# Kernel optimization log

Hardware: AMD Instinct MI355X
Metric: run time of the kernel (lower is better)

Reference implementation:

```python
import jax, jax.numpy as jnp
import numpy as np

# Uniform batched-graph layout: B graphs, each with N_PER nodes and E_PER edges.
# Graph g owns nodes [g*N_PER, (g+1)*N_PER) and edges [g*E_PER, (g+1)*E_PER).
B = 256
N_PER = 512
E_PER = 4096
D = 64               # emb_dim
RATIO = 0.25
K = int(RATIO * E_PER)  # edges reserved per graph (causal)


def setup_inputs() -> dict:
    key = jax.random.key(0)
    k_h, k_src, k_dst, k_w1, k_w2 = jax.random.split(key, 5)
    h = jax.random.normal(k_h, (B * N_PER, D), dtype=jnp.float32)
    # edge endpoints local to each graph, then offset into the global node space
    src = jax.random.randint(k_src, (B, E_PER), 0, N_PER, dtype=jnp.int32)
    dst = jax.random.randint(k_dst, (B, E_PER), 0, N_PER, dtype=jnp.int32)
    offs = (jnp.arange(B, dtype=jnp.int32) * N_PER)[:, None]
    edge_index = jnp.stack([(src + offs).reshape(-1), (dst + offs).reshape(-1)])  # [2, B*E_PER]
    batch = jnp.repeat(jnp.arange(B, dtype=jnp.int32), N_PER)  # node -> graph id
    W1 = jax.random.normal(k_w1, (2 * D, 4 * D), dtype=jnp.float32) / np.sqrt(2 * D)
    b1 = jnp.zeros((4 * D,), dtype=jnp.float32)
    W2 = jax.random.normal(k_w2, (4 * D, 1), dtype=jnp.float32) / np.sqrt(4 * D)
    b2 = jnp.zeros((1,), dtype=jnp.float32)
    return {"h": h, "W1": W1, "b1": b1, "W2": W2, "b2": b2,
            "edge_index": edge_index, "batch": batch}


def reference(h, W1, b1, W2, b2, edge_index, batch):
    row, col = edge_index[0], edge_index[1]
    # edge attention MLP: Linear(2D->4D) -> ReLU -> Linear(4D->1)
    edge_rep = jnp.concatenate([h[row], h[col]], axis=-1)          # [E, 2D]
    scores = (jax.nn.relu(edge_rep @ W1 + b1) @ W2 + b2)[:, 0]     # [E] pred_edge_weight

    # segmented top-k per graph (replaces the per-graph CPU argpartition loop)
    s = scores.reshape(B, E_PER)
    order = jnp.argsort(-s, axis=1)                                # descending
    keep = order[:, :K]                                            # causal edge slots
    drop = order[:, K:]                                            # spurious edge slots
    goff = (jnp.arange(B, dtype=keep.dtype) * E_PER)[:, None]
    keep_g = (keep + goff).reshape(-1)                             # [B*K] global edge ids
    drop_g = (drop + goff).reshape(-1)                             # [B*(E_PER-K)]
    causal_edge_weight = scores[keep_g]
    spu_edge_weight = -scores[drop_g]

    # relabel + 'feat' branch with c_pool='add': nodes touched by causal edges,
    # global_add_pool of their embeddings per graph (compaction is index-preserving math)
    ce_row = row[keep_g]
    ce_col = col[keep_g]
    node_mask = jnp.zeros((h.shape[0],), dtype=bool)
    node_mask = node_mask.at[ce_row].set(True).at[ce_col].set(True)
    causal_rep = jax.ops.segment_sum(
        jnp.where(node_mask[:, None], h, jnp.zeros((), h.dtype)),
        batch, num_segments=B)                                     # [B, D]

    return causal_rep, causal_edge_weight, spu_edge_weight
```

## Files before the change

kernel.cpp:

```cpp
#include <hip/hip_runtime.h>
#include <stdint.h>

#define B_GRAPHS 256
#define NPER     512
#define EPER     4096
#define DDIM     64
#define KKEEP    1024
#define HIDDEN   256
#define CT       16
#define NTILE    (HIDDEN/CT)
#define STR      20

__global__ __launch_bounds__(1024) void scores_kernel(
    const float* __restrict__ h, const float* __restrict__ W1,
    const float* __restrict__ b1, const float* __restrict__ W2,
    const float* __restrict__ b2, const int* __restrict__ edge0,
    const int* __restrict__ edge1, float* __restrict__ sc_out)
{
  __shared__ __align__(16) float At[NPER * STR];
  __shared__ __align__(16) float Bt[NPER * STR];
  const int t  = threadIdx.x;
  const int b  = blockIdx.x;
  const int n  = t & (NPER - 1);
  const int ch = __builtin_amdgcn_readfirstlane(t >> 9);

  int epk[4];
  float eacc[4];
#pragma unroll
  for (int i = 0; i < 4; ++i) {
    const size_t e = (size_t)b * EPER + t + i * 1024;
    epk[i] = (edge0[e] & (NPER - 1)) | ((edge1[e] & (NPER - 1)) << 16);
    eacc[i] = 0.f;
  }

  const float* __restrict__ hrow = h + ((size_t)b * NPER + n) * DDIM;

  for (int jt = 0; jt < NTILE; ++jt) {
    const int j0 = jt * CT;
    const int jc = j0 + ch * 8;

    asm volatile("" ::: "memory");

    float pa[8], pb[8];
#pragma unroll
    for (int jj = 0; jj < 8; ++jj) { pa[jj] = b1[jc + jj]; pb[jj] = 0.f; }

#pragma unroll
    for (int dc = 0; dc < 4; ++dc) {
      const float4* hp = (const float4*)(hrow + dc * 16);
      float4 h0 = hp[0], h1 = hp[1], h2 = hp[2], h3 = hp[3];
      float hc[16];
      hc[0]=h0.x; hc[1]=h0.y; hc[2]=h0.z; hc[3]=h0.w;
      hc[4]=h1.x; hc[5]=h1.y; hc[6]=h1.z; hc[7]=h1.w;
      hc[8]=h2.x; hc[9]=h2.y; hc[10]=h2.z; hc[11]=h2.w;
      hc[12]=h3.x; hc[13]=h3.y; hc[14]=h3.z; hc[15]=h3.w;
#pragma unroll
      for (int k = 0; k < 16; ++k) {
        const int d = dc * 16 + k;
        const float hv = hc[k];
#pragma unroll
        for (int jj = 0; jj < 8; ++jj)
          pa[jj] = fmaf(hv, W1[d * HIDDEN + jc + jj], pa[jj]);
#pragma unroll
        for (int jj = 0; jj < 8; ++jj)
          pb[jj] = fmaf(hv, W1[(DDIM + d) * HIDDEN + jc + jj], pb[jj]);
      }
    }

    {
      float* ap = At + n * STR + ch * 8;
      float* bp = Bt + n * STR + ch * 8;
      float4 s0 = {pa[0], pa[1], pa[2], pa[3]};
      float4 s1 = {pa[4], pa[5], pa[6], pa[7]};
      ((float4*)ap)[0] = s0; ((float4*)ap)[1] = s1;
      float4 u0 = {pb[0], pb[1], pb[2], pb[3]};
      float4 u1 = {pb[4], pb[5], pb[6], pb[7]};
      ((float4*)bp)[0] = u0; ((float4*)bp)[1] = u1;
    }
    __syncthreads();

    float w2r[CT];
#pragma unroll
    for (int jj = 0; jj < CT; ++jj) w2r[jj] = W2[j0 + jj];

#pragma unroll
    for (int i = 0; i < 4; ++i) {
      const int er = epk[i] & 0xffff;
      const int ec = ((unsigned)epk[i]) >> 16;
      const float4* ar = (const float4*)(At + er * STR);
      const float4* br = (const float4*)(Bt + ec * STR);
      float p = 0.f;
#pragma unroll
      for (int q = 0; q < 4; ++q) {
        const float4 a = ar[q], c = br[q];
        p = fmaf(fmaxf(a.x + c.x, 0.f), w2r[4*q+0], p);
        p = fmaf(fmaxf(a.y + c.y, 0.f), w2r[4*q+1], p);
        p = fmaf(fmaxf(a.z + c.z, 0.f), w2r[4*q+2], p);
        p = fmaf(fmaxf(a.w + c.w, 0.f), w2r[4*q+3], p);
      }
      eacc[i] += p;
    }
    __syncthreads();
  }

  const float b2v = b2[0];
#pragma unroll
  for (int i = 0; i < 4; ++i)
    sc_out[(size_t)b * EPER + t + i * 1024] = eacc[i] + b2v;
}

__global__ __launch_bounds__(1024) void sort_kernel(
    const float* __restrict__ sc, const int* __restrict__ edge0,
    const int* __restrict__ edge1, const float* __restrict__ h,
    float* __restrict__ out_rep, float* __restrict__ out_cw,
    float* __restrict__ out_sw)
{
  __shared__ unsigned long long keys[EPER];
  __shared__ int mask[NPER];
  __shared__ float red[16 * 64];
  const int t = threadIdx.x;
  const int b = blockIdx.x;

  if (t < NPER) mask[t] = 0;

#pragma unroll
  for (int i = 0; i < 4; ++i) {
    const int e = t + i * 1024;
    const float s = sc[(size_t)b * EPER + e];
    unsigned u  = __float_as_uint(s);
    unsigned fk = (u & 0x80000000u) ? ~u : (u | 0x80000000u);
    unsigned dk = ~fk;
    keys[e] = ((unsigned long long)dk << 32) | (unsigned)e;
  }

  for (int k = 2; k <= EPER; k <<= 1) {
    for (int j = k >> 1; j > 0; j >>= 1) {
      __syncthreads();
#pragma unroll
      for (int i = 0; i < 4; ++i) {
        const int p = t + i * 1024;
        const int l = p ^ j;
        if (l > p) {
          const unsigned long long a = keys[p], c = keys[l];
          const bool up = ((p & k) == 0);
          if (up ? (a > c) : (a < c)) { keys[p] = c; keys[l] = a; }
        }
      }
    }
  }
  __syncthreads();

#pragma unroll
  for (int i = 0; i < 4; ++i) {
    const int p = t + i * 1024;
    const unsigned long long key = keys[p];
    const unsigned fk = ~(unsigned)(key >> 32);
    const unsigned u  = (fk & 0x80000000u) ? (fk & 0x7fffffffu) : ~fk;
    const float s = __uint_as_float(u);
    if (p < KKEEP) out_cw[(size_t)b * KKEEP + p] = s;
    else           out_sw[(size_t)b * (EPER - KKEEP) + (p - KKEEP)] = -s;
  }

  {
    const int e = (int)(keys[t] & 0xffffffffu);
    const size_t eg = (size_t)b * EPER + e;
    mask[edge0[eg] & (NPER - 1)] = 1;
    mask[edge1[eg] & (NPER - 1)] = 1;
  }
  __syncthreads();

  {
    const int d = t & 63, g = t >> 6;
    float s = 0.f;
    for (int nn = g; nn < NPER; nn += 16)
      if (mask[nn]) s += h[((size_t)b * NPER + nn) * DDIM + d];
    red[g * 64 + d] = s;
  }
  __syncthreads();
  if (t < 64) {
    float tot = 0.f;
#pragma unroll
    for (int g = 0; g < 16; ++g) tot += red[g * 64 + t];
    out_rep[(size_t)b * DDIM + t] = tot;
  }
}

extern "C" void kernel_launch(void* const* d_in, const int* in_sizes, int n_in,
                              void* d_out, int out_size, void* d_ws, size_t ws_size,
                              hipStream_t stream) {
  const float* h    = (const float*)d_in[0];
  const float* W1   = (const float*)d_in[1];
  const float* b1   = (const float*)d_in[2];
  const float* W2   = (const float*)d_in[3];
  const float* b2   = (const float*)d_in[4];
  const int*   eidx = (const int*)d_in[5];
  const int* edge0 = eidx;
  const int* edge1 = eidx + (size_t)B_GRAPHS * EPER;

  float* sc = (float*)d_ws;

  float* out     = (float*)d_out;
  float* out_rep = out;
  float* out_cw  = out + B_GRAPHS * DDIM;
  float* out_sw  = out_cw + (size_t)B_GRAPHS * KKEEP;

  scores_kernel<<<B_GRAPHS, 1024, 0, stream>>>(h, W1, b1, W2, b2, edge0, edge1, sc);
  sort_kernel<<<B_GRAPHS, 1024, 0, stream>>>(sc, edge0, edge1, h, out_rep, out_cw, out_sw);
}
```

Baseline: 335.4 us.

## Warp-specialize score kernel into producer/consumer roles with double-buffered LDS

The 1024-thread block now splits into two roles. Threads 0-511 compute node projections for an 8-wide hidden tile into one of two LDS buffers, while threads 512-1023 consume the previous tile to accumulate edge scores for 8 edges each. This aims to overlap the projection FMAs with the LDS gather/ReLU work and halve the barriers per tile. In exchange each role does twice as many tiles or edges serially, and the number of pipeline ticks doubles, so per-role work and latency could rise.

```diff
diff --git a/kernel.cpp b/kernel.cpp
--- a/kernel.cpp
+++ b/kernel.cpp
@@ -7,9 +7,9 @@
 #define DDIM     64
 #define KKEEP    1024
 #define HIDDEN   256
-#define CT       16
-#define NTILE    (HIDDEN/CT)
-#define STR      20
+#define CT       8
+#define NTICK    (HIDDEN/CT)
+#define STR      12
 
 __global__ __launch_bounds__(1024) void scores_kernel(
     const float* __restrict__ h, const float* __restrict__ W1,
@@ -17,96 +17,99 @@
     const float* __restrict__ b2, const int* __restrict__ edge0,
     const int* __restrict__ edge1, float* __restrict__ sc_out)
 {
-  __shared__ __align__(16) float At[NPER * STR];
-  __shared__ __align__(16) float Bt[NPER * STR];
-  const int t  = threadIdx.x;
-  const int b  = blockIdx.x;
-  const int n  = t & (NPER - 1);
-  const int ch = __builtin_amdgcn_readfirstlane(t >> 9);
-
-  int epk[4];
-  float eacc[4];
-#pragma unroll
-  for (int i = 0; i < 4; ++i) {
-    const size_t e = (size_t)b * EPER + t + i * 1024;
-    epk[i] = (edge0[e] & (NPER - 1)) | ((edge1[e] & (NPER - 1)) << 16);
-    eacc[i] = 0.f;
+  __shared__ __align__(16) float At[2][NPER * STR];
+  __shared__ __align__(16) float Bt[2][NPER * STR];
+  const int t    = threadIdx.x;
+  const int b    = blockIdx.x;
+  const int role = __builtin_amdgcn_readfirstlane(t >> 9);
+  const int n    = t & (NPER - 1);
+
+  int epk[8];
+  float eacc[8];
+  if (role) {
+#pragma unroll
+    for (int i = 0; i < 8; ++i) {
+      const size_t e = (size_t)b * EPER + n + i * 512;
+      epk[i]  = (edge0[e] & (NPER - 1)) | ((edge1[e] & (NPER - 1)) << 16);
+      eacc[i] = 0.f;
+    }
   }
 
   const float* __restrict__ hrow = h + ((size_t)b * NPER + n) * DDIM;
 
-  for (int jt = 0; jt < NTILE; ++jt) {
-    const int j0 = jt * CT;
-    const int jc = j0 + ch * 8;
-
-    asm volatile("" ::: "memory");
-
-    float pa[8], pb[8];
-#pragma unroll
-    for (int jj = 0; jj < 8; ++jj) { pa[jj] = b1[jc + jj]; pb[jj] = 0.f; }
-
-#pragma unroll
-    for (int dc = 0; dc < 4; ++dc) {
-      const float4* hp = (const float4*)(hrow + dc * 16);
-      float4 h0 = hp[0], h1 = hp[1], h2 = hp[2], h3 = hp[3];
-      float hc[16];
-      hc[0]=h0.x; hc[1]=h0.y; hc[2]=h0.z; hc[3]=h0.w;
-      hc[4]=h1.x; hc[5]=h1.y; hc[6]=h1.z; hc[7]=h1.w;
-      hc[8]=h2.x; hc[9]=h2.y; hc[10]=h2.z; hc[11]=h2.w;
-      hc[12]=h3.x; hc[13]=h3.y; hc[14]=h3.z; hc[15]=h3.w;
-#pragma unroll
-      for (int k = 0; k < 16; ++k) {
-        const int d = dc * 16 + k;
-        const float hv = hc[k];
-#pragma unroll
-        for (int jj = 0; jj < 8; ++jj)
-          pa[jj] = fmaf(hv, W1[d * HIDDEN + jc + jj], pa[jj]);
-#pragma unroll
-        for (int jj = 0; jj < 8; ++jj)
-          pb[jj] = fmaf(hv, W1[(DDIM + d) * HIDDEN + jc + jj], pb[jj]);
+  for (int jt = 0; jt <= NTICK; ++jt) {
+    if (role == 0) {
+      if (jt < NTICK) {
+        const int jc = jt * CT;
+        asm volatile("" ::: "memory");
+        float pa[CT], pb[CT];
+#pragma unroll
+        for (int jj = 0; jj < CT; ++jj) { pa[jj] = b1[jc + jj]; pb[jj] = 0.f; }
+#pragma unroll
+        for (int dc = 0; dc < 4; ++dc) {
+          const float4* hp = (const float4*)(hrow + dc * 16);
+          const float4 h0 = hp[0], h1 = hp[1], h2 = hp[2], h3 = hp[3];
+          const float hc[16] = {h0.x,h0.y,h0.z,h0.w, h1.x,h1.y,h1.z,h1.w,
+                                h2.x,h2.y,h2.z,h2.w, h3.x,h3.y,h3.z,h3.w};
+#pragma unroll
+          for (int k = 0; k < 16; ++k) {
+            const int d = dc * 16 + k;
+            const float hv = hc[k];
+#pragma unroll
+            for (int jj = 0; jj < CT; ++jj)
+              pa[jj] = fmaf(hv, W1[d * HIDDEN + jc + jj], pa[jj]);
+#pragma unroll
+            for (int jj = 0; jj < CT; ++jj)
+              pb[jj] = fmaf(hv, W1[(DDIM + d) * HIDDEN + jc + jj], pb[jj]);
+          }
+        }
+        const int p = jt & 1;
+        float4 s0 = {pa[0], pa[1], pa[2], pa[3]};
+        float4 s1 = {pa[4], pa[5], pa[6], pa[7]};
+        ((float4*)(At[p] + n * STR))[0] = s0;
+        ((float4*)(At[p] + n * STR))[1] = s1;
+        float4 u0 = {pb[0], pb[1], pb[2], pb[3]};
+        float4 u1 = {pb[4], pb[5], pb[6], pb[7]};
+        ((float4*)(Bt[p] + n * STR))[0] = u0;
+        ((float4*)(Bt[p] + n * STR))[1] = u1;
+      }
+    } else {
+      if (jt >= 1) {
+        const int jc = (jt - 1) * CT;
+        const int p  = (jt - 1) & 1;
+        float w2r[CT];
+#pragma unroll
+        for (int jj = 0; jj < CT; ++jj) w2r[jj] = W2[jc + jj];
+#pragma unroll
+        for (int i = 0; i < 8; ++i) {
+          const int er = epk[i] & 0xffff;
+          const int ec = ((unsigned)epk[i]) >> 16;
+          const float4* ar = (const float4*)(At[p] + er * STR);
+          const float4* br = (const float4*)(Bt[p] + ec * STR);
+          const float4 a0 = ar[0], a1 = ar[1];
+          const float4 c0 = br[0], c1 = br[1];
+          float q = 0.f;
+          q = fmaf(fmaxf(a0.x + c0.x, 0.f), w2r[0], q);
+          q = fmaf(fmaxf(a0.y + c0.y, 0.f), w2r[1], q);
+          q = fmaf(fmaxf(a0.z + c0.z, 0.f), w2r[2], q);
+          q = fmaf(fmaxf(a0.w + c0.w, 0.f), w2r[3], q);
+          q = fmaf(fmaxf(a1.x + c1.x, 0.f), w2r[4], q);
+          q = fmaf(fmaxf(a1.y + c1.y, 0.f), w2r[5], q);
+          q = fmaf(fmaxf(a1.z + c1.z, 0.f), w2r[6], q);
+          q = fmaf(fmaxf(a1.w + c1.w, 0.f), w2r[7], q);
+          eacc[i] += q;
+        }
       }
     }
-
-    {
-      float* ap = At + n * STR + ch * 8;
-      float* bp = Bt + n * STR + ch * 8;
-      float4 s0 = {pa[0], pa[1], pa[2], pa[3]};
-      float4 s1 = {pa[4], pa[5], pa[6], pa[7]};
-      ((float4*)ap)[0] = s0; ((float4*)ap)[1] = s1;
-      float4 u0 = {pb[0], pb[1], pb[2], pb[3]};
-      float4 u1 = {pb[4], pb[5], pb[6], pb[7]};
-      ((float4*)bp)[0] = u0; ((float4*)bp)[1] = u1;
-    }
     __syncthreads();
-
-    float w2r[CT];
-#pragma unroll
-    for (int jj = 0; jj < CT; ++jj) w2r[jj] = W2[j0 + jj];
-
-#pragma unroll
-    for (int i = 0; i < 4; ++i) {
-      const int er = epk[i] & 0xffff;
-      const int ec = ((unsigned)epk[i]) >> 16;
-      const float4* ar = (const float4*)(At + er * STR);
-      const float4* br = (const float4*)(Bt + ec * STR);
-      float p = 0.f;
-#pragma unroll
-      for (int q = 0; q < 4; ++q) {
-        const float4 a = ar[q], c = br[q];
-        p = fmaf(fmaxf(a.x + c.x, 0.f), w2r[4*q+0], p);
-        p = fmaf(fmaxf(a.y + c.y, 0.f), w2r[4*q+1], p);
-        p = fmaf(fmaxf(a.z + c.z, 0.f), w2r[4*q+2], p);
-        p = fmaf(fmaxf(a.w + c.w, 0.f), w2r[4*q+3], p);
-      }
-      eacc[i] += p;
-    }
-    __syncthreads();
-  }
-
-  const float b2v = b2[0];
-#pragma unroll
-  for (int i = 0; i < 4; ++i)
-    sc_out[(size_t)b * EPER + t + i * 1024] = eacc[i] + b2v;
+  }
+
+  if (role) {
+    const float b2v = b2[0];
+#pragma unroll
+    for (int i = 0; i < 8; ++i)
+      sc_out[(size_t)b * EPER + n + i * 512] = eacc[i] + b2v;
+  }
 }
 
 __global__ __launch_bounds__(1024) void sort_kernel(
```

After: 362.2 us. 1.08x slower.

## Double-buffer hidden-column tiles and halve tile width in scores kernel

Applied to the files above, without the earlier changes.

Splits the hidden dimension into 8-column tiles instead of 16 and double-buffers the per-node partial projections in shared memory. Each iteration computes the next tile while the edges consume the previous one, so only one barrier per iteration remains instead of two. The cost is twice as many tile iterations, each reloading h rows and doing fewer FMAs, and a smaller per-thread register tile.

```diff
diff --git a/kernel.cpp b/kernel.cpp
--- a/kernel.cpp
+++ b/kernel.cpp
@@ -7,9 +7,11 @@
 #define DDIM     64
 #define KKEEP    1024
 #define HIDDEN   256
-#define CT       16
+#define CT       8
 #define NTILE    (HIDDEN/CT)
-#define STR      20
+#define STR      12
+
+typedef unsigned long long u64;
 
 __global__ __launch_bounds__(1024) void scores_kernel(
     const float* __restrict__ h, const float* __restrict__ W1,
@@ -17,8 +19,8 @@
     const float* __restrict__ b2, const int* __restrict__ edge0,
     const int* __restrict__ edge1, float* __restrict__ sc_out)
 {
-  __shared__ __align__(16) float At[NPER * STR];
-  __shared__ __align__(16) float Bt[NPER * STR];
+  __shared__ __align__(16) float At[2][NPER * STR];
+  __shared__ __align__(16) float Bt[2][NPER * STR];
   const int t  = threadIdx.x;
   const int b  = blockIdx.x;
   const int n  = t & (NPER - 1);
@@ -35,71 +37,73 @@
 
   const float* __restrict__ hrow = h + ((size_t)b * NPER + n) * DDIM;
 
-  for (int jt = 0; jt < NTILE; ++jt) {
-    const int j0 = jt * CT;
-    const int jc = j0 + ch * 8;
-
-    asm volatile("" ::: "memory");
-
-    float pa[8], pb[8];
-#pragma unroll
-    for (int jj = 0; jj < 8; ++jj) { pa[jj] = b1[jc + jj]; pb[jj] = 0.f; }
-
-#pragma unroll
-    for (int dc = 0; dc < 4; ++dc) {
-      const float4* hp = (const float4*)(hrow + dc * 16);
-      float4 h0 = hp[0], h1 = hp[1], h2 = hp[2], h3 = hp[3];
-      float hc[16];
-      hc[0]=h0.x; hc[1]=h0.y; hc[2]=h0.z; hc[3]=h0.w;
-      hc[4]=h1.x; hc[5]=h1.y; hc[6]=h1.z; hc[7]=h1.w;
-      hc[8]=h2.x; hc[9]=h2.y; hc[10]=h2.z; hc[11]=h2.w;
-      hc[12]=h3.x; hc[13]=h3.y; hc[14]=h3.z; hc[15]=h3.w;
-#pragma unroll
-      for (int k = 0; k < 16; ++k) {
-        const int d = dc * 16 + k;
-        const float hv = hc[k];
-#pragma unroll
-        for (int jj = 0; jj < 8; ++jj)
-          pa[jj] = fmaf(hv, W1[d * HIDDEN + jc + jj], pa[jj]);
-#pragma unroll
-        for (int jj = 0; jj < 8; ++jj)
-          pb[jj] = fmaf(hv, W1[(DDIM + d) * HIDDEN + jc + jj], pb[jj]);
+  for (int jt = 0; jt <= NTILE; ++jt) {
+    if (jt < NTILE) {
+      const int cur = jt & 1;
+      const int jc  = jt * CT + ch * 4;
+
+      asm volatile("" ::: "memory");
+
+      float pa[4], pb[4];
+#pragma unroll
+      for (int jj = 0; jj < 4; ++jj) { pa[jj] = b1[jc + jj]; pb[jj] = 0.f; }
+
+#pragma unroll
+      for (int dc = 0; dc < 4; ++dc) {
+        const float4* hp = (const float4*)(hrow + dc * 16);
+        float4 h0 = hp[0], h1 = hp[1], h2 = hp[2], h3 = hp[3];
+        float hc[16];
+        hc[0]=h0.x; hc[1]=h0.y; hc[2]=h0.z; hc[3]=h0.w;
+        hc[4]=h1.x; hc[5]=h1.y; hc[6]=h1.z; hc[7]=h1.w;
+        hc[8]=h2.x; hc[9]=h2.y; hc[10]=h2.z; hc[11]=h2.w;
+        hc[12]=h3.x; hc[13]=h3.y; hc[14]=h3.z; hc[15]=h3.w;
+#pragma unroll
+        for (int k = 0; k < 16; ++k) {
+          const int d = dc * 16 + k;
+          const float hv = hc[k];
+#pragma unroll
+          for (int jj = 0; jj < 4; ++jj)
+            pa[jj] = fmaf(hv, W1[d * HIDDEN + jc + jj], pa[jj]);
+#pragma unroll
+          for (int jj = 0; jj < 4; ++jj)
+            pb[jj] = fmaf(hv, W1[(DDIM + d) * HIDDEN + jc + jj], pb[jj]);
+        }
+      }
+      {
+        float4 s = {pa[0], pa[1], pa[2], pa[3]};
+        float4 u = {pb[0], pb[1], pb[2], pb[3]};
+        *(float4*)(At[cur] + n * STR + ch * 4) = s;
+        *(float4*)(Bt[cur] + n * STR + ch * 4) = u;
       }
     }
 
-    {
-      float* ap = At + n * STR + ch * 8;
-      float* bp = Bt + n * STR + ch * 8;
-      float4 s0 = {pa[0], pa[1], pa[2], pa[3]};
-      float4 s1 = {pa[4], pa[5], pa[6], pa[7]};
-      ((float4*)ap)[0] = s0; ((float4*)ap)[1] = s1;
-      float4 u0 = {pb[0], pb[1], pb[2], pb[3]};
-      float4 u1 = {pb[4], pb[5], pb[6], pb[7]};
-      ((float4*)bp)[0] = u0; ((float4*)bp)[1] = u1;
+    if (jt >= 1) {
+      const int p  = (jt - 1) & 1;
+      const int j0 = (jt - 1) * CT;
+      float w2r[CT];
+#pragma unroll
+      for (int jj = 0; jj < CT; ++jj) w2r[jj] = W2[j0 + jj];
+#pragma unroll
+      for (int i = 0; i < 4; ++i) {
+        const int er = epk[i] & 0xffff;
+        const int ec = ((unsigned)epk[i]) >> 16;
+        const float4* ar = (const float4*)(At[p] + er * STR);
+        const float4* br = (const float4*)(Bt[p] + ec * STR);
+        const float4 a0 = ar[0], a1 = ar[1];
+        const float4 c0 = br[0], c1 = br[1];
+        float q = 0.f;
+        q = fmaf(fmaxf(a0.x + c0.x, 0.f), w2r[0], q);
+        q = fmaf(fmaxf(a0.y + c0.y, 0.f), w2r[1], q);
+        q = fmaf(fmaxf(a0.z + c0.z, 0.f), w2r[2], q);
+        q = fmaf(fmaxf(a0.w + c0.w, 0.f), w2r[3], q);
+        q = fmaf(fmaxf(a1.x + c1.x, 0.f), w2r[4], q);
+        q = fmaf(fmaxf(a1.y + c1.y, 0.f), w2r[5], q);
+        q = fmaf(fmaxf(a1.z + c1.z, 0.f), w2r[6], q);
+        q = fmaf(fmaxf(a1.w + c1.w, 0.f), w2r[7], q);
+        eacc[i] += q;
+      }
     }
-    __syncthreads();
-
-    float w2r[CT];
-#pragma unroll
-    for (int jj = 0; jj < CT; ++jj) w2r[jj] = W2[j0 + jj];
-
-#pragma unroll
-    for (int i = 0; i < 4; ++i) {
-      const int er = epk[i] & 0xffff;
-      const int ec = ((unsigned)epk[i]) >> 16;
-      const float4* ar = (const float4*)(At + er * STR);
-      const float4* br = (const float4*)(Bt + ec * STR);
-      float p = 0.f;
-#pragma unroll
-      for (int q = 0; q < 4; ++q) {
-        const float4 a = ar[q], c = br[q];
-        p = fmaf(fmaxf(a.x + c.x, 0.f), w2r[4*q+0], p);
-        p = fmaf(fmaxf(a.y + c.y, 0.f), w2r[4*q+1], p);
-        p = fmaf(fmaxf(a.z + c.z, 0.f), w2r[4*q+2], p);
-        p = fmaf(fmaxf(a.w + c.w, 0.f), w2r[4*q+3], p);
-      }
-      eacc[i] += p;
-    }
+
     __syncthreads();
   }
 
```

After: 406.8 us. 21.3% more time.
